# Kernel tuning notes

Hardware: AMD Instinct MI355X
Metric: run time of the kernel (lower is better)

The kernel has to match this reference:

```python
import jax, jax.numpy as jnp
import numpy as np
from jax import lax

B, D, N, K, POOL = 256, 512, 50000, 32, 1024
ALPHA, BETA, LAMB = 1.0, 1.0, 1e-4
TAU, EPS, DELTA = 0.1, 0.1, 1e-3
SINKHORN_ITERS = 200


def matrix_sqrt(A):
    # differentiable symmetric PSD matrix sqrt via eigendecomposition
    w, v = jnp.linalg.eigh(A)
    w = jnp.clip(w, 0.0)
    return (v * jnp.sqrt(w)) @ v.T


def ridge_cov(M, delta):
    Dm = M.shape[0]
    S = M + (jnp.trace(M) / Dm * delta) * jnp.eye(Dm, dtype=M.dtype)
    return 0.5 * (S + S.T)


def sinkhorn(p, q, C, eps):
    # entropic OT, fixed-iteration Sinkhorn (ot.sinkhorn equivalent)
    Kmat = jnp.exp(-C / eps)
    def step(uv, _):
        u, v = uv
        u = p / (Kmat @ v + 1e-16)
        v = q / (Kmat.T @ u + 1e-16)
        return (u, v), None
    (u, v), _ = lax.scan(step, (jnp.ones_like(p), jnp.ones_like(q)), None, length=SINKHORN_ITERS)
    return u[:, None] * Kmat * v[None, :]


def setup_inputs():
    key = jax.random.key(0)
    k1, k2, k3, k4, k5, k6 = jax.random.split(key, 6)
    return {
        "q_batch": jax.random.normal(k1, (B, D), jnp.float32),
        "q_indices": jax.random.randint(k2, (B,), 0, POOL),
        "W": jax.random.normal(k3, (D, D), jnp.float32) * 0.05,
        "X": jax.random.normal(k4, (N, D), jnp.float32),
        "pre_indices": jax.random.randint(k5, (POOL, K), 0, N),
        "pre_weights": jax.random.uniform(k6, (POOL, K), jnp.float32, 0.1, 1.0),
    }


def _forward(q_batch, W, X, pre_weights, q_indices, pre_indices):
    T = q_batch @ W  # model := single linear layer, T_q_batch [B, D]
    # ---- distribution alignment (2-Wasserstein between Gaussians) ----
    mu_X = X.mean(0)
    Sigma_X = ridge_cov(jnp.cov(X, rowvar=False).astype(X.dtype), DELTA)
    mu_t = T.mean(0)
    Sigma_t = ridge_cov(jnp.cov(T, rowvar=False).astype(T.dtype), max(DELTA, 1e-4))
    term_mean = jnp.sum((mu_t - mu_X) ** 2)
    s_t = matrix_sqrt(Sigma_t)
    M = s_t @ Sigma_X @ s_t
    s_m = matrix_sqrt(0.5 * (M + M.T))
    term_cov = jnp.trace(Sigma_X + Sigma_t - 2.0 * s_m)
    loss_dist = term_mean + jnp.clip(term_cov, 0.0)
    # ---- kNN consistency with entropic OT ----
    T_sg = lax.stop_gradient(T)  # faiss search is on detached queries
    d2 = (T_sg ** 2).sum(1, keepdims=True) - 2.0 * T_sg @ X.T + (X ** 2).sum(1)[None, :]
    _, post_idx = lax.top_k(-d2, K)  # exact brute-force kNN == faiss IndexFlatL2
    Xn = X[post_idx]  # [B, K, D]
    l2 = ((T[:, None, :] - Xn) ** 2).sum(-1)  # [B, K], grads flow through T
    post_w = jax.nn.softmax(-l2 / TAU, axis=1)
    post_w = jnp.clip(post_w, 1e-8)
    post_w = post_w / post_w.sum(1, keepdims=True)
    pre_idx_b = pre_indices[q_indices]  # [B, K]
    pre_w = jnp.clip(pre_weights[q_indices], 1e-8)
    pre_w = pre_w / pre_w.sum(1, keepdims=True)
    # fixed-size support = concat(pre, post) of size 2K; duplicated points cost 0
    # to move between, so OT value matches the deduped-union formulation
    support = jnp.concatenate([pre_idx_b, post_idx], axis=1)  # [B, 2K]
    S = X[support]  # [B, 2K, D]
    sq = (S ** 2).sum(-1)
    C = jnp.clip(sq[:, :, None] + sq[:, None, :] - 2.0 * jnp.einsum('bid,bjd->bij', S, S), 0.0)
    med = jnp.median(C.reshape(C.shape[0], -1), axis=1)
    C = C / (med[:, None, None] + 1e-8)
    zeros = jnp.zeros_like(pre_w)
    p = jnp.concatenate([pre_w, zeros], axis=1)   # pre mass on first K slots
    q = jnp.concatenate([zeros, post_w], axis=1)  # post mass on last K slots
    plans = jax.vmap(lambda pp, qq, cc: sinkhorn(pp, qq, cc, EPS))(p, q, C)
    loss_knn = (plans * C).sum((1, 2)).mean()
    loss_reg = 0.5 * jnp.sum(W ** 2)
    total = ALPHA * loss_dist + BETA * loss_knn + LAMB * loss_reg
    return total, loss_dist, loss_knn


def reference(q_batch, q_indices, W, X, pre_indices, pre_weights):
    return _forward(q_batch, W, X, pre_weights, q_indices, pre_indices)
```

## Files before the change

### kernel.cpp

```cpp
#include <hip/hip_runtime.h>
#include <float.h>
#include <math.h>

#define BB 256
#define DD 512
#define NN 50000
#define KK 32
#define NS_ITERS 11
#define PARTS 8
#define PCH 6250

#define OFF_G     0
#define OFF_SC    262144
#define OFF_CS    262208
#define OFF_CSS   262720
#define ZERO_F    263232
#define OFF_T     263232
#define OFF_TC    394304
#define OFF_P     525376
#define OFF_H     656448
#define OFF_XSQ   723008
#define OFF_RUNI  781200
#define OFF_PW    789392
#define OFF_PRW   797584
#define OFF_D2    805776

#define OFF_UUT   (OFF_G)
#define OFF_TCTC  (OFF_G + 65536)
#define OFF_W     (OFF_G + 131072)
#define OFF_M     (OFF_G + 131328)
#define OFF_MUT   (OFF_G + 200000)

typedef __attribute__((ext_vector_type(8))) short bf16x8;
typedef __attribute__((ext_vector_type(4))) float f32x4;

__device__ __forceinline__ float waveSum(float v) {
#pragma unroll
  for (int off = 32; off > 0; off >>= 1) v += __shfl_xor(v, off);
  return v;
}

__device__ __forceinline__ void cvt_write(float4 v, unsigned short* hi, unsigned short* lo, int sa) {
  unsigned int b0 = __float_as_uint(v.x), b1 = __float_as_uint(v.y);
  unsigned int b2 = __float_as_uint(v.z), b3 = __float_as_uint(v.w);
  unsigned int h0 = b0 & 0xffff0000u, h1 = b1 & 0xffff0000u;
  unsigned int h2 = b2 & 0xffff0000u, h3 = b3 & 0xffff0000u;
  float l0 = v.x - __uint_as_float(h0), l1 = v.y - __uint_as_float(h1);
  float l2 = v.z - __uint_as_float(h2), l3 = v.w - __uint_as_float(h3);
  *(unsigned int*)&hi[sa]     = (h0 >> 16) | h1;
  *(unsigned int*)&hi[sa + 2] = (h2 >> 16) | h3;
  *(unsigned int*)&lo[sa]     = (__float_as_uint(l0) >> 16) | (__float_as_uint(l1) & 0xffff0000u);
  *(unsigned int*)&lo[sa + 2] = (__float_as_uint(l2) >> 16) | (__float_as_uint(l3) & 0xffff0000u);
}

__device__ __forceinline__ void cvt1(float x, unsigned short* hp, unsigned short* lp) {
  unsigned int bb = __float_as_uint(x);
  unsigned int hb = bb & 0xffff0000u;
  float lo = x - __uint_as_float(hb);
  *hp = (unsigned short)(hb >> 16);
  *lp = (unsigned short)(__float_as_uint(lo) >> 16);
}

__global__ void __launch_bounds__(256) k_g64_nn(const float* __restrict__ A,
                                                const float* __restrict__ B,
                                                float* __restrict__ C,
                                                int K, int lda, int ldb, int ldc, float scale) {
  __shared__ float As[64][65], Bs[64][65];
  int m0 = blockIdx.y * 64, n0 = blockIdx.x * 64;
  int t = threadIdx.x, tr = t >> 4, tc = t & 15;
  float acc[4][4] = {{0.f}};
  for (int k0 = 0; k0 < K; k0 += 64) {
#pragma unroll
    for (int p = 0; p < 16; ++p) {
      int l = t + 256 * p;
      int r = l >> 6, c = l & 63;
      As[r][c] = A[(m0 + r) * lda + k0 + c];
      Bs[r][c] = B[(k0 + r) * ldb + n0 + c];
    }
    __syncthreads();
#pragma unroll 16
    for (int kk = 0; kk < 64; ++kk) {
      float a[4], b[4];
#pragma unroll
      for (int u = 0; u < 4; ++u) a[u] = As[tr + 16 * u][kk];
#pragma unroll
      for (int v = 0; v < 4; ++v) b[v] = Bs[kk][tc + 16 * v];
#pragma unroll
      for (int u = 0; u < 4; ++u)
#pragma unroll
        for (int v = 0; v < 4; ++v) acc[u][v] += a[u] * b[v];
    }
    __syncthreads();
  }
#pragma unroll
  for (int u = 0; u < 4; ++u)
#pragma unroll
    for (int v = 0; v < 4; ++v)
      C[(m0 + tr + 16 * u) * ldc + n0 + tc + 16 * v] = acc[u][v] * scale;
}

__global__ void __launch_bounds__(256) k_g64_nt(const float* __restrict__ A,
                                                const float* __restrict__ B,
                                                float* __restrict__ C,
                                                int K, int lda, int ldb, int ldc, float scale) {
  __shared__ float As[64][65], Bs[64][65];
  int m0 = blockIdx.y * 64, n0 = blockIdx.x * 64;
  int t = threadIdx.x, tr = t >> 4, tc = t & 15;
  float acc[4][4] = {{0.f}};
  for (int k0 = 0; k0 < K; k0 += 64) {
#pragma unroll
    for (int p = 0; p < 16; ++p) {
      int l = t + 256 * p;
      int r = l >> 6, c = l & 63;
      As[r][c] = A[(m0 + r) * lda + k0 + c];
      Bs[r][c] = B[(n0 + r) * ldb + k0 + c];
    }
    __syncthreads();
#pragma unroll 16
    for (int kk = 0; kk < 64; ++kk) {
      float a[4], b[4];
#pragma unroll
      for (int u = 0; u < 4; ++u) a[u] = As[tr + 16 * u][kk];
#pragma unroll
      for (int v = 0; v < 4; ++v) b[v] = Bs[tc + 16 * v][kk];
#pragma unroll
      for (int u = 0; u < 4; ++u)
#pragma unroll
        for (int v = 0; v < 4; ++v) acc[u][v] += a[u] * b[v];
    }
    __syncthreads();
  }
#pragma unroll
  for (int u = 0; u < 4; ++u)
#pragma unroll
    for (int v = 0; v < 4; ++v)
      C[(m0 + tr + 16 * u) * ldc + n0 + tc + 16 * v] = acc[u][v] * scale;
}

__global__ void __launch_bounds__(256) k_vgemm(const float* __restrict__ T,
                                               const float* __restrict__ X,
                                               float* __restrict__ V) {
  __shared__ unsigned short Ah[128 * 72], Al[128 * 72], Bh[128 * 72], Bl[128 * 72];
  int bj = blockIdx.x, bi = blockIdx.y;
  int t = threadIdx.x;
  int wave = t >> 6, lane = t & 63;
  int m0 = (wave >> 1) * 64, n0 = (wave & 1) * 64;
  int lrow = lane & 15, lq = lane >> 4;
  f32x4 acc[4][4] = {};
  for (int kc = 0; kc < 512; kc += 64) {
#pragma unroll
    for (int f = 0; f < 8; ++f) {
      int lin = f * 256 + t;
      int r = lin >> 4, c4 = lin & 15;
      int sa = r * 72 + c4 * 4;
      float4 va = *(const float4*)&T[(bi * 128 + r) * 512 + kc + c4 * 4];
      cvt_write(va, Ah, Al, sa);
      int jg = bj * 128 + r;
      float4 vb = {0.f, 0.f, 0.f, 0.f};
      if (jg < NN) vb = *(const float4*)&X[(size_t)jg * 512 + kc + c4 * 4];
      cvt_write(vb, Bh, Bl, sa);
    }
    __syncthreads();
#pragma unroll
    for (int ks = 0; ks < 2; ++ks) {
      int kb = ks * 32 + lq * 8;
      bf16x8 ah[4], al[4], bh[4], bl[4];
#pragma unroll
      for (int mi = 0; mi < 4; ++mi) {
        int ro = (m0 + mi * 16 + lrow) * 72 + kb;
        ah[mi] = *(const bf16x8*)&Ah[ro];
        al[mi] = *(const bf16x8*)&Al[ro];
      }
#pragma unroll
      for (int nj = 0; nj < 4; ++nj) {
        int ro = (n0 + nj * 16 + lrow) * 72 + kb;
        bh[nj] = *(const bf16x8*)&Bh[ro];
        bl[nj] = *(const bf16x8*)&Bl[ro];
      }
#pragma unroll
      for (int mi = 0; mi < 4; ++mi)
#pragma unroll
        for (int nj = 0; nj < 4; ++nj) {
          acc[mi][nj] = __builtin_amdgcn_mfma_f32_16x16x32_bf16(ah[mi], bh[nj], acc[mi][nj], 0, 0, 0);
          acc[mi][nj] = __builtin_amdgcn_mfma_f32_16x16x32_bf16(ah[mi], bl[nj], acc[mi][nj], 0, 0, 0);
          acc[mi][nj] = __builtin_amdgcn_mfma_f32_16x16x32_bf16(al[mi], bh[nj], acc[mi][nj], 0, 0, 0);
        }
    }
    __syncthreads();
  }
#pragma unroll
  for (int mi = 0; mi < 4; ++mi)
#pragma unroll
    for (int nj = 0; nj < 4; ++nj)
#pragma unroll
      for (int r = 0; r < 4; ++r) {
        int row = bi * 128 + m0 + mi * 16 + lq * 4 + r;
        int col = bj * 128 + n0 + nj * 16 + lrow;
        if (col < NN) V[(size_t)row * NN + col] = acc[mi][nj][r];
      }
}

__global__ void __launch_bounds__(256) k_uut(const float* __restrict__ V,
                                             const float* __restrict__ m,
                                             float* __restrict__ UUT) {
  __shared__ unsigned short Ah[128 * 72], Al[128 * 72], Bh[128 * 72], Bl[128 * 72];
  const int pi_[3] = {0, 0, 1}, pj_[3] = {0, 1, 1};
  int bi = pi_[blockIdx.x], bj = pj_[blockIdx.x];
  int j0 = blockIdx.y * 1000, jlim = j0 + 1000;
  int t = threadIdx.x;
  int wave = t >> 6, lane = t & 63;
  int m0 = (wave >> 1) * 64, n0 = (wave & 1) * 64;
  int lrow = lane & 15, lq = lane >> 4;
  f32x4 acc[4][4] = {};
  for (int ch = 0; ch < 16; ++ch) {
    int jc = j0 + ch * 64;
#pragma unroll
    for (int f = 0; f < 8; ++f) {
      int lin = f * 256 + t;
      int r = lin >> 4, c4 = lin & 15;
      int sa = r * 72 + c4 * 4;
      int jb = jc + c4 * 4;
      float4 va = {0.f, 0.f, 0.f, 0.f}, vb = {0.f, 0.f, 0.f, 0.f};
      if (jb < jlim) {
        float4 mm = *(const float4*)&m[jb];
        va = *(const float4*)&V[(size_t)(bi * 128 + r) * NN + jb];
        vb = *(const float4*)&V[(size_t)(bj * 128 + r) * NN + jb];
        va.x -= mm.x; va.y -= mm.y; va.z -= mm.z; va.w -= mm.w;
        vb.x -= mm.x; vb.y -= mm.y; vb.z -= mm.z; vb.w -= mm.w;
      }
      cvt_write(va, Ah, Al, sa);
      cvt_write(vb, Bh, Bl, sa);
    }
    __syncthreads();
#pragma unroll
    for (int ks = 0; ks < 2; ++ks) {
      int kb = ks * 32 + lq * 8;
      bf16x8 ah[4], al[4], bh[4], bl[4];
#pragma unroll
      for (int mi = 0; mi < 4; ++mi) {
        int ro = (m0 + mi * 16 + lrow) * 72 + kb;
        ah[mi] = *(const bf16x8*)&Ah[ro];
        al[mi] = *(const bf16x8*)&Al[ro];
      }
#pragma unroll
      for (int nj = 0; nj < 4; ++nj) {
        int ro = (n0 + nj * 16 + lrow) * 72 + kb;
        bh[nj] = *(const bf16x8*)&Bh[ro];
        bl[nj] = *(const bf16x8*)&Bl[ro];
      }
#pragma unroll
      for (int mi = 0; mi < 4; ++mi)
#pragma unroll
        for (int nj = 0; nj < 4; ++nj) {
          acc[mi][nj] = __builtin_amdgcn_mfma_f32_16x16x32_bf16(ah[mi], bh[nj], acc[mi][nj], 0, 0, 0);
          acc[mi][nj] = __builtin_amdgcn_mfma_f32_16x16x32_bf16(ah[mi], bl[nj], acc[mi][nj], 0, 0, 0);
          acc[mi][nj] = __builtin_amdgcn_mfma_f32_16x16x32_bf16(al[mi], bh[nj], acc[mi][nj], 0, 0, 0);
        }
    }
    __syncthreads();
  }
#pragma unroll
  for (int mi = 0; mi < 4; ++mi)
#pragma unroll
    for (int nj = 0; nj < 4; ++nj)
#pragma unroll
      for (int r = 0; r < 4; ++r) {
        int row = bi * 128 + m0 + mi * 16 + lq * 4 + r;
        int col = bj * 128 + n0 + nj * 16 + lrow;
        atomicAdd(&UUT[row * 256 + col], acc[mi][nj][r]);
      }
}

__global__ void __launch_bounds__(256) k_colstatX(const float* __restrict__ X, float* __restrict__ colsum,
                                                  float* __restrict__ colss) {
  __shared__ float shs[512], shss[512];
  int b = blockIdx.x, t = threadIdx.x;
  int c4 = (t & 127) * 4, g = t >> 7;
  int r0 = b * 200 + g;
  float sx = 0, sy = 0, sz = 0, sw = 0;
  float qx = 0, qy = 0, qz = 0, qw = 0;
#pragma unroll 4
  for (int it = 0; it < 100; ++it) {
    float4 v = *(const float4*)&X[(size_t)(r0 + 2 * it) * 512 + c4];
    sx += v.x; sy += v.y; sz += v.z; sw += v.w;
    qx += v.x * v.x; qy += v.y * v.y; qz += v.z * v.z; qw += v.w * v.w;
  }
  if (g == 1) {
    int o = (t - 128) * 4;
    shs[o] = sx; shs[o + 1] = sy; shs[o + 2] = sz; shs[o + 3] = sw;
    shss[o] = qx; shss[o + 1] = qy; shss[o + 2] = qz; shss[o + 3] = qw;
  }
  __syncthreads();
  if (g == 0) {
    int o = t * 4;
    atomicAdd(&colsum[c4],     sx + shs[o]);
    atomicAdd(&colsum[c4 + 1], sy + shs[o + 1]);
    atomicAdd(&colsum[c4 + 2], sz + shs[o + 2]);
    atomicAdd(&colsum[c4 + 3], sw + shs[o + 3]);
    atomicAdd(&colss[c4],     qx + shss[o]);
    atomicAdd(&colss[c4 + 1], qy + shss[o + 1]);
    atomicAdd(&colss[c4 + 2], qz + shss[o + 2]);
    atomicAdd(&colss[c4 + 3], qw + shss[o + 3]);
  }
}

__global__ void k_xsq(const float* __restrict__ X, float* __restrict__ xsq) {
  int row = blockIdx.x * 4 + (threadIdx.x >> 6);
  int lane = threadIdx.x & 63;
  const float* Xr = X + (size_t)row * 512;
  float s = 0.f;
#pragma unroll
  for (int d = 0; d < 8; ++d) { float v = Xr[lane + 64 * d]; s += v * v; }
  s = waveSum(s);
  if (lane == 0) xsq[row] = s;
}

__global__ void k_colmeanT(const float* __restrict__ T, float* __restrict__ mu) {
  int c = threadIdx.x;
  int r0 = blockIdx.x * 16;
  float s = 0.f;
#pragma unroll
  for (int r = 0; r < 16; ++r) s += T[(r0 + r) * 512 + c];
  atomicAdd(&mu[c], s);
}

__global__ void k_centerT(const float* __restrict__ T, const float* __restrict__ mu,
                          float* __restrict__ Tc, float* __restrict__ scal) {
  __shared__ float red[4];
  int t = threadIdx.x;
  int base = blockIdx.x * 1024;
  float ss = 0.f;
#pragma unroll
  for (int p = 0; p < 4; ++p) {
    int l = base + p * 256 + t;
    float v = T[l] - mu[l & 511] * (1.0f / 256.0f);
    Tc[l] = v;
    ss += v * v;
  }
  ss = waveSum(ss);
  if ((t & 63) == 0) red[t >> 6] = ss;
  __syncthreads();
  if (t == 0) atomicAdd(&scal[0], red[0] + red[1] + red[2] + red[3]);
}

__global__ void k_trCX(const float* __restrict__ colsum, const float* __restrict__ colss,
                       float* __restrict__ scal) {
  __shared__ float red[8];
  int t = threadIdx.x;
  float mu = colsum[t] * (1.0f / 50000.0f);
  float v = (colss[t] - 50000.0f * mu * mu) * (1.0f / 49999.0f);
  v = waveSum(v);
  if ((t & 63) == 0) red[t >> 6] = v;
  __syncthreads();
  if (t == 0) {
    float s = 0;
    for (int i = 0; i < 8; ++i) s += red[i];
    scal[1] = s;
  }
}

__global__ void k_vstats(const float* __restrict__ V, float* __restrict__ m) {
  int j = blockIdx.x * 256 + threadIdx.x;
  if (j >= NN) return;
  int i0 = blockIdx.y * 32;
  float s = 0.f;
#pragma unroll 8
  for (int i = 0; i < 32; ++i) s += V[(size_t)(i0 + i) * NN + j];
  atomicAdd(&m[j], s * (1.0f / 256.0f));
}

__global__ void __launch_bounds__(256) k_wvec(const float* __restrict__ T,
                                              const float* __restrict__ colsum,
                                              float* __restrict__ w, float* __restrict__ scal) {
  __shared__ float cs[512];
  int t = threadIdx.x, lane = t & 63, wv_ = t >> 6;
  cs[t] = colsum[t] * (1.0f / 50000.0f);
  cs[t + 256] = colsum[t + 256] * (1.0f / 50000.0f);
  __syncthreads();
  int rbase = blockIdx.x * 32 + wv_ * 8;
  float tot = 0.f;
  for (int rr = 0; rr < 8; ++rr) {
    int row = rbase + rr;
    float a = 0.f;
#pragma unroll
    for (int d = 0; d < 8; ++d) a += T[row * 512 + lane + 64 * d] * cs[lane + 64 * d];
    a = waveSum(a);
    if (lane == 0) { w[row] = a; tot += a; }
  }
  if (lane == 0) atomicAdd(&scal[6], tot);
}

__global__ void k_hfix(const float* __restrict__ UUT, const float* __restrict__ TcTc,
                       const float* __restrict__ w, const float* __restrict__ scal,
                       float* __restrict__ H) {
  int l = blockIdx.x * 256 + threadIdx.x;
  int i = l >> 8, j = l & 255;
  float u = (i >= 128 && j < 128) ? UUT[j * 256 + i] : UUT[i * 256 + j];
  float rho = scal[1] * (1e-3f / 512.0f);
  float wm = scal[6] * (1.0f / 256.0f);
  float wi = w[i] - wm, wj = w[j] - wm;
  H[l] = (u - 50000.0f * wi * wj) * (1.0f / (49999.0f * 255.0f))
       + rho * TcTc[i * 256 + j] * (1.0f / 255.0f);
}

__global__ void __launch_bounds__(256) k_power(const float* __restrict__ H,
                                               float* __restrict__ scal) {
  __shared__ float v[256], nv[256], red[4];
  int t = threadIdx.x;
  float rt = scal[0] * (1.0f / 255.0f) * (1e-3f / 512.0f);
  v[t] = 1.0f;
  __syncthreads();
  float n2 = 256.0f, n3 = 256.0f;
  for (int it = 0; it < 3; ++it) {
    float s = rt * v[t];
    for (int j = 0; j < 256; ++j) s += H[t * 256 + j] * v[j];
    nv[t] = s;
    float ss = waveSum(s * s);
    if ((t & 63) == 0) red[t >> 6] = ss;
    __syncthreads();
    float norm2 = red[0] + red[1] + red[2] + red[3];
    if (it == 1) n2 = norm2;
    if (it == 2) n3 = norm2;
    v[t] = nv[t];
    __syncthreads();
  }
  float d = H[t * 256 + t] + rt;
#pragma unroll
  for (int off = 32; off > 0; off >>= 1) d = fmaxf(d, __shfl_xor(d, off));
  if ((t & 63) == 0) red[t >> 6] = d;
  __syncthreads();
  if (t == 0) {
    float lam = sqrtf(n3 / n2);
    float md = fmaxf(fmaxf(red[0], red[1]), fmaxf(red[2], red[3]));
    scal[5] = fmaxf(1.3f * lam, md);
  }
}

__global__ void k_nsinit(const float* __restrict__ H, const float* __restrict__ scal,
                         float* __restrict__ Y, float* __restrict__ Z) {
  int l = blockIdx.x * 256 + threadIdx.x;
  int i = l >> 8, j = l & 255;
  float rt = scal[0] * (1.0f / 255.0f) * (1e-3f / 512.0f);
  float inv = 1.0f / scal[5];
  Y[l] = (H[l] + ((i == j) ? rt : 0.f)) * inv;
  Z[l] = (i == j) ? 1.0f : 0.f;
}

__global__ void __launch_bounds__(256) k_nsp(const float* __restrict__ Z,
                                             const float* __restrict__ Y,
                                             float* __restrict__ P) {
  __shared__ unsigned short Ah[64 * 72], Al[64 * 72], Bh[64 * 72], Bl[64 * 72];
  int n0b = blockIdx.x * 64, m0b = blockIdx.y * 64;
  int t = threadIdx.x, wave = t >> 6, lane = t & 63;
  int m0 = (wave >> 1) * 32, n0 = (wave & 1) * 32;
  int lrow = lane & 15, lq = lane >> 4;
  f32x4 acc[2][2] = {};
  for (int k0 = 0; k0 < 256; k0 += 64) {
#pragma unroll
    for (int f = 0; f < 4; ++f) {
      int lin = f * 256 + t;
      int r = lin >> 4, c4 = (lin & 15) * 4;
      float4 va = *(const float4*)&Z[(m0b + r) * 256 + k0 + c4];
      cvt_write(va, Ah, Al, r * 72 + c4);
      float4 vb = *(const float4*)&Y[(k0 + r) * 256 + n0b + c4];
      cvt1(vb.x, &Bh[(c4 + 0) * 72 + r], &Bl[(c4 + 0) * 72 + r]);
      cvt1(vb.y, &Bh[(c4 + 1) * 72 + r], &Bl[(c4 + 1) * 72 + r]);
      cvt1(vb.z, &Bh[(c4 + 2) * 72 + r], &Bl[(c4 + 2) * 72 + r]);
      cvt1(vb.w, &Bh[(c4 + 3) * 72 + r], &Bl[(c4 + 3) * 72 + r]);
    }
    __syncthreads();
#pragma unroll
    for (int ks = 0; ks < 2; ++ks) {
      int kb = ks * 32 + lq * 8;
      bf16x8 ah[2], al2[2], bh[2], bl2[2];
#pragma unroll
      for (int mi = 0; mi < 2; ++mi) {
        int ro = (m0 + mi * 16 + lrow) * 72 + kb;
        ah[mi] = *(const bf16x8*)&Ah[ro];
        al2[mi] = *(const bf16x8*)&Al[ro];
      }
#pragma unroll
      for (int nj = 0; nj < 2; ++nj) {
        int ro = (n0 + nj * 16 + lrow) * 72 + kb;
        bh[nj] = *(const bf16x8*)&Bh[ro];
        bl2[nj] = *(const bf16x8*)&Bl[ro];
      }
#pragma unroll
      for (int mi = 0; mi < 2; ++mi)
#pragma unroll
        for (int nj = 0; nj < 2; ++nj) {
          acc[mi][nj] = __builtin_amdgcn_mfma_f32_16x16x32_bf16(ah[mi], bh[nj], acc[mi][nj], 0, 0, 0);
          acc[mi][nj] = __builtin_amdgcn_mfma_f32_16x16x32_bf16(ah[mi], bl2[nj], acc[mi][nj], 0, 0, 0);
          acc[mi][nj] = __builtin_amdgcn_mfma_f32_16x16x32_bf16(al2[mi], bh[nj], acc[mi][nj], 0, 0, 0);
        }
    }
    __syncthreads();
  }
#pragma unroll
  for (int mi = 0; mi < 2; ++mi)
#pragma unroll
    for (int nj = 0; nj < 2; ++nj)
#pragma unroll
      for (int r = 0; r < 4; ++r) {
        int row = m0b + m0 + mi * 16 + lq * 4 + r;
        int col = n0b + n0 + nj * 16 + lrow;
        P[row * 256 + col] = acc[mi][nj][r];
      }
}

__global__ void __launch_bounds__(256) k_nsu(const float* __restrict__ Y, const float* __restrict__ Z,
                                             const float* __restrict__ Pm,
                                             float* __restrict__ Yn, float* __restrict__ Zn) {
  __shared__ unsigned short Ah[64 * 72], Al[64 * 72], Bh[64 * 72], Bl[64 * 72];
  int zz = blockIdx.z;
  const float* A = zz ? Pm : Y;
  const float* B = zz ? Z : Pm;
  const float* D = zz ? Z : Y;
  float* O = zz ? Zn : Yn;
  int n0b = blockIdx.x * 64, m0b = blockIdx.y * 64;
  int t = threadIdx.x, wave = t >> 6, lane = t & 63;
  int m0 = (wave >> 1) * 32, n0 = (wave & 1) * 32;
  int lrow = lane & 15, lq = lane >> 4;
  f32x4 acc[2][2] = {};
  for (int k0 = 0; k0 < 256; k0 += 64) {
#pragma unroll
    for (int f = 0; f < 4; ++f) {
      int lin = f * 256 + t;
      int r = lin >> 4, c4 = (lin & 15) * 4;
      float4 va = *(const float4*)&A[(m0b + r) * 256 + k0 + c4];
      cvt_write(va, Ah, Al, r * 72 + c4);
      float4 vb = *(const float4*)&B[(k0 + r) * 256 + n0b + c4];
      cvt1(vb.x, &Bh[(c4 + 0) * 72 + r], &Bl[(c4 + 0) * 72 + r]);
      cvt1(vb.y, &Bh[(c4 + 1) * 72 + r], &Bl[(c4 + 1) * 72 + r]);
      cvt1(vb.z, &Bh[(c4 + 2) * 72 + r], &Bl[(c4 + 2) * 72 + r]);
      cvt1(vb.w, &Bh[(c4 + 3) * 72 + r], &Bl[(c4 + 3) * 72 + r]);
    }
    __syncthreads();
#pragma unroll
    for (int ks = 0; ks < 2; ++ks) {
      int kb = ks * 32 + lq * 8;
      bf16x8 ah[2], al2[2], bh[2], bl2[2];
#pragma unroll
      for (int mi = 0; mi < 2; ++mi) {
        int ro = (m0 + mi * 16 + lrow) * 72 + kb;
        ah[mi] = *(const bf16x8*)&Ah[ro];
        al2[mi] = *(const bf16x8*)&Al[ro];
      }
#pragma unroll
      for (int nj = 0; nj < 2; ++nj) {
        int ro = (n0 + nj * 16 + lrow) * 72 + kb;
        bh[nj] = *(const bf16x8*)&Bh[ro];
        bl2[nj] = *(const bf16x8*)&Bl[ro];
      }
#pragma unroll
      for (int mi = 0; mi < 2; ++mi)
#pragma unroll
        for (int nj = 0; nj < 2; ++nj) {
          acc[mi][nj] = __builtin_amdgcn_mfma_f32_16x16x32_bf16(ah[mi], bh[nj], acc[mi][nj], 0, 0, 0);
          acc[mi][nj] = __builtin_amdgcn_mfma_f32_16x16x32_bf16(ah[mi], bl2[nj], acc[mi][nj], 0, 0, 0);
          acc[mi][nj] = __builtin_amdgcn_mfma_f32_16x16x32_bf16(al2[mi], bh[nj], acc[mi][nj], 0, 0, 0);
        }
    }
    __syncthreads();
  }
#pragma unroll
  for (int mi = 0; mi < 2; ++mi)
#pragma unroll
    for (int nj = 0; nj < 2; ++nj)
#pragma unroll
      for (int r = 0; r < 4; ++r) {
        int row = m0b + m0 + mi * 16 + lq * 4 + r;
        int col = n0b + n0 + nj * 16 + lrow;
        int idx = row * 256 + col;
        O[idx] = 1.5f * D[idx] - 0.5f * acc[mi][nj][r];
      }
}

__global__ void k_ns_trace(const float* __restrict__ Y, float* __restrict__ scal) {
  __shared__ float red[4];
  int t = threadIdx.x;
  float v = Y[t * 256 + t];
  v = waveSum(v);
  if ((t & 63) == 0) red[t >> 6] = v;
  __syncthreads();
  if (t == 0) {
    float tr = red[0] + red[1] + red[2] + red[3];
    float rt = scal[0] * (1.0f / 255.0f) * (1e-3f / 512.0f);
    scal[2] = sqrtf(scal[5]) * tr + 256.0f * sqrtf(rt);
  }
}

__global__ void __launch_bounds__(256) k_topk_part(const float* __restrict__ V,
                                                   const float* __restrict__ xsq,
                                                   float* __restrict__ candv,
                                                   int* __restrict__ candi) {
  __shared__ float bufv[512];
  __shared__ int bufi[512];
  __shared__ int lcount;
  __shared__ float tvs;
  __shared__ int tis;
  int part = blockIdx.x, q = blockIdx.y, t = threadIdx.x;
  int base = part * PCH;
  int lane = t & 63;
  if (t == 0) { lcount = 0; tvs = FLT_MAX; tis = 0x7fffffff; }
  __syncthreads();
  const float* rowV = V + (size_t)q * NN + base;
  const float* xs = xsq + base;

  auto flush = [&]() {
    __syncthreads();
    int c = lcount;
    for (int s = c + t; s < 512; s += 256) { bufv[s] = FLT_MAX; bufi[s] = 0x7fffffff; }
    __syncthreads();
    for (int ssz = 2; ssz <= 512; ssz <<= 1) {
      for (int st = ssz >> 1; st > 0; st >>= 1) {
        int i = 2 * t - (t & (st - 1));
        int j = i + st;
        bool up = ((i & ssz) == 0);
        float a = bufv[i], b = bufv[j];
        int ai = bufi[i], bi2 = bufi[j];
        bool agtb = (a > b) || (a == b && ai > bi2);
        if (agtb == up) { bufv[i] = b; bufv[j] = a; bufi[i] = bi2; bufi[j] = ai; }
        __syncthreads();
      }
    }
    if (t == 0) { lcount = 32; tvs = bufv[31]; tis = bufi[31]; }
    __syncthreads();
  };

  int ntile = (PCH + 255) >> 8;
  for (int tile = 0; tile < ntile; ++tile) {
    int j = tile * 256 + t;
    float val = 0.f; int idx = 0;
    bool pred = false;
    if (j < PCH) {
      val = xs[j] - 2.0f * rowV[j];
      idx = base + j;
      float tv = tvs; int ti = tis;
      pred = (val < tv) || (val == tv && idx < ti);
    }
    unsigned long long mask = __ballot(pred);
    if (mask) {
      int lead = __ffsll((unsigned long long)mask) - 1;
      int cnt = __popcll(mask);
      int basep = 0;
      if (lane == lead) basep = atomicAdd(&lcount, cnt);
      basep = __shfl(basep, lead);
      if (pred) {
        int off = __popcll(mask & ((1ull << lane) - 1ull));
        int slot = basep + off;
        bufv[slot] = val; bufi[slot] = idx;
      }
    }
    __syncthreads();
    if (lcount >= 256) flush();
  }
  flush();
  if (t < 32) {
    candv[(q * PARTS + part) * 32 + t] = bufv[t];
    candi[(q * PARTS + part) * 32 + t] = bufi[t];
  }
}

__global__ void __launch_bounds__(128) k_topk_final(const float* __restrict__ candv,
                                                    const int* __restrict__ candi,
                                                    int* __restrict__ runi) {
  __shared__ float v[256];
  __shared__ int ix[256];
  int q = blockIdx.x, t = threadIdx.x;
  v[t] = candv[q * 256 + t];
  v[t + 128] = candv[q * 256 + t + 128];
  ix[t] = candi[q * 256 + t];
  ix[t + 128] = candi[q * 256 + t + 128];
  __syncthreads();
  for (int ssz = 2; ssz <= 256; ssz <<= 1) {
    for (int st = ssz >> 1; st > 0; st >>= 1) {
      int i = 2 * t - (t & (st - 1));
      int j = i + st;
      bool up = ((i & ssz) == 0);
      float a = v[i], b = v[j];
      int ai = ix[i], bi = ix[j];
      bool agtb = (a > b) || (a == b && ai > bi);
      if (agtb == up) { v[i] = b; v[j] = a; ix[i] = bi; ix[j] = ai; }
      __syncthreads();
    }
  }
  if (t < 32) runi[q * 32 + t] = ix[t];
}

__global__ void __launch_bounds__(64) k_l2soft(const float* __restrict__ T, const float* __restrict__ X,
                                               const int* __restrict__ runi, const int* __restrict__ qidx,
                                               const float* __restrict__ prew, float* __restrict__ postw,
                                               float* __restrict__ prewn) {
  __shared__ float l2s[32];
  int b = blockIdx.x, lane = threadIdx.x;
  int qi = qidx[b];
  float pwv = (lane < 32) ? fmaxf(prew[qi * 32 + lane], 1e-8f) : 0.f;
  float psum = waveSum(pwv);
  if (lane < 32) prewn[b * 32 + lane] = pwv / psum;
  const float* Tb = T + b * 512;
  for (int n = 0; n < 32; ++n) {
    int nb = runi[b * 32 + n];
    const float* Xr = X + (size_t)nb * 512;
    float acc = 0.f;
#pragma unroll
    for (int d = 0; d < 8; ++d) {
      float df = Tb[lane + 64 * d] - Xr[lane + 64 * d];
      acc += df * df;
    }
    acc = waveSum(acc);
    if (lane == 0) l2s[n] = acc;
  }
  __syncthreads();
  float lg = (lane < 32) ? (-l2s[lane] * 10.0f) : -FLT_MAX;
  float mx = lg;
#pragma unroll
  for (int off = 32; off > 0; off >>= 1) mx = fmaxf(mx, __shfl_xor(mx, off));
  float e = (lane < 32) ? expf(lg - mx) : 0.f;
  float es = waveSum(e);
  float wv = e / es;
  wv = fmaxf(wv, 1e-8f);
  float ws2 = (lane < 32) ? wv : 0.f;
  ws2 = waveSum(ws2);
  if (lane < 32) postw[b * 32 + lane] = wv / ws2;
}

__global__ void __launch_bounds__(256) k_batch(const float* __restrict__ X, const int* __restrict__ qidx,
                                               const int* __restrict__ pre_idx, const int* __restrict__ runi,
                                               const float* __restrict__ prewn, const float* __restrict__ postw,
                                               float* __restrict__ scal) {
  __shared__ float G[64][65];
  __shared__ float Cm[64][65];
  __shared__ unsigned short Ah[64 * 72], Al[64 * 72];
  __shared__ int supp[64];
  __shared__ float uuS[32], vvS[32];
  __shared__ float red[4];
  __shared__ float medsh;
  __shared__ unsigned int hist[256];
  __shared__ unsigned int wtot[4];
  __shared__ unsigned int selp;
  __shared__ int selk;
  __shared__ unsigned int cw[4], mw[4];
  int b = blockIdx.x, t = threadIdx.x;
  int wave = t >> 6, lane = t & 63;
  if (t < 32) supp[t] = pre_idx[qidx[b] * 32 + t];
  else if (t < 64) supp[t] = runi[b * 32 + t - 32];
  if (t == 0) { selp = 0u; selk = 992; }
  __syncthreads();
  {
    int m0 = (wave >> 1) * 32, n0 = (wave & 1) * 32;
    int lrow = lane & 15, lq = lane >> 4;
    f32x4 acc[2][2] = {};
    for (int kc = 0; kc < 512; kc += 64) {
#pragma unroll
      for (int f = 0; f < 4; ++f) {
        int lin = f * 256 + t;
        int r = lin >> 4, c4 = lin & 15;
        float4 va = *(const float4*)&X[(size_t)supp[r] * 512 + kc + c4 * 4];
        cvt_write(va, Ah, Al, r * 72 + c4 * 4);
      }
      __syncthreads();
#pragma unroll
      for (int ks = 0; ks < 2; ++ks) {
        int kb = ks * 32 + lq * 8;
        bf16x8 ah[2], al[2], bh[2], bl[2];
#pragma unroll
        for (int mi = 0; mi < 2; ++mi) {
          int ro = (m0 + mi * 16 + lrow) * 72 + kb;
          ah[mi] = *(const bf16x8*)&Ah[ro];
          al[mi] = *(const bf16x8*)&Al[ro];
        }
#pragma unroll
        for (int nj = 0; nj < 2; ++nj) {
          int ro = (n0 + nj * 16 + lrow) * 72 + kb;
          bh[nj] = *(const bf16x8*)&Ah[ro];
          bl[nj] = *(const bf16x8*)&Al[ro];
        }
#pragma unroll
        for (int mi = 0; mi < 2; ++mi)
#pragma unroll
          for (int nj = 0; nj < 2; ++nj) {
            acc[mi][nj] = __builtin_amdgcn_mfma_f32_16x16x32_bf16(ah[mi], bh[nj], acc[mi][nj], 0, 0, 0);
            acc[mi][nj] = __builtin_amdgcn_mfma_f32_16x16x32_bf16(ah[mi], bl[nj], acc[mi][nj], 0, 0, 0);
            acc[mi][nj] = __builtin_amdgcn_mfma_f32_16x16x32_bf16(al[mi], bh[nj], acc[mi][nj], 0, 0, 0);
          }
      }
      __syncthreads();
    }
#pragma unroll
    for (int mi = 0; mi < 2; ++mi)
#pragma unroll
      for (int nj = 0; nj < 2; ++nj)
#pragma unroll
        for (int r = 0; r < 4; ++r)
          G[m0 + mi * 16 + lq * 4 + r][n0 + nj * 16 + lrow] = acc[mi][nj][r];
  }
  __syncthreads();
  for (int l = t; l < 4096; l += 256) {
    int i = l >> 6, j = l & 63;
    Cm[i][j] = fmaxf(G[i][i] + G[j][j] - 2.0f * G[i][j], 0.f);
  }
  __syncthreads();
  for (int pass = 0; pass < 4; ++pass) {
    int shift = 24 - 8 * pass;
    hist[t] = 0u;
    __syncthreads();
    for (int l = t; l < 4096; l += 256) {
      int i = l >> 6, j = l & 63;
      if (i < j) {
        unsigned int u = __float_as_uint(Cm[i][j]) & 0x7fffffffu;
        bool match = (pass == 0) || (((u ^ selp) >> (shift + 8)) == 0u);
        if (match) atomicAdd(&hist[(u >> shift) & 255], 1u);
      }
    }
    __syncthreads();
    unsigned int h = hist[t];
    unsigned int c = h;
#pragma unroll
    for (int off = 1; off < 64; off <<= 1) {
      unsigned int n = __shfl_up(c, off);
      if ((t & 63) >= off) c += n;
    }
    if ((t & 63) == 63) wtot[t >> 6] = c;
    __syncthreads();
    unsigned int offw = 0;
    for (int w2 = 0; w2 < (t >> 6); ++w2) offw += wtot[w2];
    c += offw;
    int k = selk;
    if ((int)c >= k && (int)(c - h) < k) {
      selk = k - (int)(c - h);
      selp = selp | ((unsigned int)t << shift);
    }
    __syncthreads();
  }
  {
    unsigned int target = selp;
    unsigned int cnt = 0, mn = 0xffffffffu;
    for (int l = t; l < 4096; l += 256) {
      int i = l >> 6, j = l & 63;
      if (i < j) {
        unsigned int u = __float_as_uint(Cm[i][j]) & 0x7fffffffu;
        if (u <= target) cnt++;
        else mn = (u < mn) ? u : mn;
      }
    }
#pragma unroll
    for (int off = 32; off > 0; off >>= 1) {
      cnt += __shfl_xor(cnt, off);
      unsigned int m2 = __shfl_xor(mn, off);
      mn = (m2 < mn) ? m2 : mn;
    }
    if (lane == 0) { cw[wave] = cnt; mw[wave] = mn; }
    __syncthreads();
    if (t == 0) {
      unsigned int ct = cw[0] + cw[1] + cw[2] + cw[3];
      unsigned int mt = mw[0];
      mt = (mw[1] < mt) ? mw[1] : mt;
      mt = (mw[2] < mt) ? mw[2] : mt;
      mt = (mw[3] < mt) ? mw[3] : mt;
      float v992 = __uint_as_float(target);
      float v993 = (ct >= 993u) ? v992 : __uint_as_float(mt);
      medsh = 0.5f * (v992 + v993) + 1e-8f;
    }
    __syncthreads();
  }
  float inv = 1.0f / medsh;
  for (int l = t; l < 4096; l += 256) {
    int i = l >> 6, j = l & 63;
    float cn = Cm[i][j] * inv;
    Cm[i][j] = cn;
    G[i][j] = expf(-cn * 10.0f);
  }
  __syncthreads();
  if (wave == 0) {
    int half = lane >> 5;
    int l = lane & 31;
    int cb = half * 16;
    float p_l = prewn[b * 32 + l];
    float q_l = postw[b * 32 + l];
    float Kr16[16], Kt16[16];
#pragma unroll
    for (int c2 = 0; c2 < 16; ++c2) Kr16[c2] = G[l][32 + cb + c2];
#pragma unroll
    for (int r2 = 0; r2 < 16; ++r2) Kt16[r2] = G[cb + r2][32 + l];
    float r0 = 0.f;
#pragma unroll
    for (int c2 = 0; c2 < 32; ++c2) r0 += G[l][half * 32 + c2];
    r0 += __shfl_xor(r0, 32);
    float u = p_l / (r0 + 1e-16f);
    float s0 = 0.f, s1 = 0.f, s2 = 0.f, s3 = 0.f;
#pragma unroll
    for (int r2 = 0; r2 < 16; r2 += 4) {
      s0 += Kt16[r2]     * __shfl(u, cb + r2);
      s1 += Kt16[r2 + 1] * __shfl(u, cb + r2 + 1);
      s2 += Kt16[r2 + 2] * __shfl(u, cb + r2 + 2);
      s3 += Kt16[r2 + 3] * __shfl(u, cb + r2 + 3);
    }
    float sv = (s0 + s1) + (s2 + s3);
    sv += __shfl_xor(sv, 32);
    float v = q_l / (sv + 1e-16f);
    for (int it = 1; it < 200; ++it) {
      float uprev = u, vprev = v;
      float a0 = 0.f, a1 = 0.f, a2 = 0.f, a3 = 0.f;
#pragma unroll
      for (int c2 = 0; c2 < 16; c2 += 4) {
        a0 += Kr16[c2]     * __shfl(v, cb + c2);
        a1 += Kr16[c2 + 1] * __shfl(v, cb + c2 + 1);
        a2 += Kr16[c2 + 2] * __shfl(v, cb + c2 + 2);
        a3 += Kr16[c2 + 3] * __shfl(v, cb + c2 + 3);
      }
      float au = (a0 + a1) + (a2 + a3);
      au += __shfl_xor(au, 32);
      u = p_l / (au + 1e-16f);
      a0 = 0.f; a1 = 0.f; a2 = 0.f; a3 = 0.f;
#pragma unroll
      for (int r2 = 0; r2 < 16; r2 += 4) {
        a0 += Kt16[r2]     * __shfl(u, cb + r2);
        a1 += Kt16[r2 + 1] * __shfl(u, cb + r2 + 1);
        a2 += Kt16[r2 + 2] * __shfl(u, cb + r2 + 2);
        a3 += Kt16[r2 + 3] * __shfl(u, cb + r2 + 3);
      }
      float bv = (a0 + a1) + (a2 + a3);
      bv += __shfl_xor(bv, 32);
      v = q_l / (bv + 1e-16f);
      if (__all(u == uprev && v == vprev)) break;
    }
    if (t < 32) { uuS[t] = u; vvS[t] = v; }
  }
  __syncthreads();
  float lacc = 0.f;
#pragma unroll
  for (int q8 = 0; q8 < 4; ++q8) {
    int l = q8 * 256 + t;
    int i = l >> 5, j = l & 31;
    lacc += uuS[i] * G[i][32 + j] * vvS[j] * Cm[i][32 + j];
  }
  lacc = waveSum(lacc);
  if ((t & 63) == 0) red[t >> 6] = lacc;
  __syncthreads();
  if (t == 0)
    atomicAdd(&scal[3], (red[0] + red[1] + red[2] + red[3]) * (1.0f / 256.0f));
}

__global__ void k_wreg(const float* __restrict__ W, float* __restrict__ scal) {
  __shared__ float red[4];
  int t = threadIdx.x;
  int base = blockIdx.x * 2048;
  float ss = 0.f;
#pragma unroll
  for (int p = 0; p < 8; ++p) {
    float v = W[base + p * 256 + t];
    ss += v * v;
  }
  ss = waveSum(ss);
  if ((t & 63) == 0) red[t >> 6] = ss;
  __syncthreads();
  if (t == 0) atomicAdd(&scal[4], red[0] + red[1] + red[2] + red[3]);
}

__global__ void k_combine(const float* __restrict__ mu_t, const float* __restrict__ colsum,
                          const float* __restrict__ scal, float* __restrict__ out) {
  __shared__ float red[8];
  int t = threadIdx.x;
  float dm = mu_t[t] * (1.0f / 256.0f) - colsum[t] * (1.0f / 50000.0f);
  float v = dm * dm;
  v = waveSum(v);
  if ((t & 63) == 0) red[t >> 6] = v;
  __syncthreads();
  if (t == 0) {
    float term_mean = 0.f;
    for (int i = 0; i < 8; ++i) term_mean += red[i];
    float trCT = scal[0] * (1.0f / 255.0f);
    float trCX = scal[1];
    float S = scal[2];
    float term_cov = trCX * 1.001f + trCT * 1.001f - 2.0f * S;
    term_cov = fmaxf(term_cov, 0.f);
    float loss_dist = term_mean + term_cov;
    float loss_knn = scal[3];
    float loss_reg = 0.5f * scal[4];
    out[0] = loss_dist + loss_knn + 1e-4f * loss_reg;
    out[1] = loss_dist;
    out[2] = loss_knn;
  }
}

extern "C" void kernel_launch(void* const* d_in, const int* in_sizes, int n_in,
                              void* d_out, int out_size, void* d_ws, size_t ws_size,
                              hipStream_t stream) {
  const float* q = (const float*)d_in[0];
  const int* qidx = (const int*)d_in[1];
  const float* W = (const float*)d_in[2];
  const float* X = (const float*)d_in[3];
  const int* pre_idx = (const int*)d_in[4];
  const float* prew = (const float*)d_in[5];
  float* out = (float*)d_out;
  float* ws = (float*)d_ws;

  float* scal = ws + OFF_SC;
  float* colsum = ws + OFF_CS;
  float* colss = ws + OFF_CSS;
  float* T = ws + OFF_T;
  float* Tc = ws + OFF_TC;
  float* H = ws + OFF_H;
  float* mu_t = ws + OFF_MUT;
  float* xsq = ws + OFF_XSQ;
  int* runi = (int*)(ws + OFF_RUNI);
  float* postw = ws + OFF_PW;
  float* prewn = ws + OFF_PRW;
  float* V = ws + OFF_D2;
  float* UUT = ws + OFF_UUT;
  float* TcTc = ws + OFF_TCTC;
  float* wv = ws + OFF_W;
  float* m = ws + OFF_M;
  float* candv = ws + OFF_P;
  int* candi = (int*)(ws + OFF_P + 65536);

  hipMemsetAsync(d_ws, 0, (size_t)ZERO_F * 4, stream);

  k_g64_nn<<<dim3(8, 4), 256, 0, stream>>>(q, W, T, 512, 512, 512, 512, 1.0f);
  k_colstatX<<<250, 256, 0, stream>>>(X, colsum, colss);
  k_xsq<<<12500, 256, 0, stream>>>(X, xsq);
  k_colmeanT<<<16, 512, 0, stream>>>(T, mu_t);
  k_centerT<<<128, 256, 0, stream>>>(T, mu_t, Tc, scal);
  k_trCX<<<1, 512, 0, stream>>>(colsum, colss, scal);
  k_vgemm<<<dim3(391, 2), 256, 0, stream>>>(T, X, V);
  k_vstats<<<dim3(196, 8), 256, 0, stream>>>(V, m);
  k_topk_part<<<dim3(PARTS, 256), 256, 0, stream>>>(V, xsq, candv, candi);
  k_topk_final<<<256, 128, 0, stream>>>(candv, candi, runi);
  k_g64_nt<<<dim3(4, 4), 256, 0, stream>>>(Tc, Tc, TcTc, 512, 512, 512, 256, 1.0f);
  k_wvec<<<8, 256, 0, stream>>>(T, colsum, wv, scal);
  k_uut<<<dim3(3, 50), 256, 0, stream>>>(V, m, UUT);
  k_hfix<<<256, 256, 0, stream>>>(UUT, TcTc, wv, scal, H);
  {
    float* Y = ws + OFF_TC;
    float* Z = ws + OFF_TC + 65536;
    float* Y2 = ws + OFF_P;
    float* Z2 = ws + OFF_P + 65536;
    float* Pm = ws + OFF_G;
    k_power<<<1, 256, 0, stream>>>(H, scal);
    k_nsinit<<<256, 256, 0, stream>>>(H, scal, Y, Z);
    for (int it = 0; it < NS_ITERS; ++it) {
      k_nsp<<<dim3(4, 4), 256, 0, stream>>>(Z, Y, Pm);
      k_nsu<<<dim3(4, 4, 2), 256, 0, stream>>>(Y, Z, Pm, Y2, Z2);
      float* tmp = Y; Y = Y2; Y2 = tmp;
      tmp = Z; Z = Z2; Z2 = tmp;
    }
    k_ns_trace<<<1, 256, 0, stream>>>(Y, scal);
  }
  k_l2soft<<<256, 64, 0, stream>>>(T, X, runi, qidx, prew, postw, prewn);
  k_batch<<<256, 256, 0, stream>>>(X, qidx, pre_idx, runi, prewn, postw, scal);
  k_wreg<<<128, 256, 0, stream>>>(W, scal);
  k_combine<<<1, 512, 0, stream>>>(mu_t, colsum, scal, out);
}
```

Measured before the change: 1.016 ms.

## Fuse column means into GEMM epilogues and register-prefetch next tiles in GEMMs

```diff
diff --git a/kernel.cpp b/kernel.cpp
--- a/kernel.cpp
+++ b/kernel.cpp
@@ -64,8 +64,10 @@
 __global__ void __launch_bounds__(256) k_g64_nn(const float* __restrict__ A,
                                                 const float* __restrict__ B,
                                                 float* __restrict__ C,
-                                                int K, int lda, int ldb, int ldc, float scale) {
+                                                int K, int lda, int ldb, int ldc, float scale,
+                                                float* __restrict__ musum) {
   __shared__ float As[64][65], Bs[64][65];
+  __shared__ float cp[64];
   int m0 = blockIdx.y * 64, n0 = blockIdx.x * 64;
   int t = threadIdx.x, tr = t >> 4, tc = t & 15;
   float acc[4][4] = {{0.f}};
@@ -97,6 +99,19 @@
 #pragma unroll
     for (int v = 0; v < 4; ++v)
       C[(m0 + tr + 16 * u) * ldc + n0 + tc + 16 * v] = acc[u][v] * scale;
+  if (musum != nullptr) {
+    if (t < 64) cp[t] = 0.f;
+    __syncthreads();
+#pragma unroll
+    for (int v = 0; v < 4; ++v) {
+      float s = 0.f;
+#pragma unroll
+      for (int u = 0; u < 4; ++u) s += acc[u][v];
+      atomicAdd(&cp[tc + 16 * v], s * scale);
+    }
+    __syncthreads();
+    if (t < 64) atomicAdd(&musum[n0 + t], cp[t]);
+  }
 }
 
 __global__ void __launch_bounds__(256) k_g64_nt(const float* __restrict__ A,
@@ -139,28 +154,47 @@
 
 __global__ void __launch_bounds__(256) k_vgemm(const float* __restrict__ T,
                                                const float* __restrict__ X,
-                                               float* __restrict__ V) {
+                                               float* __restrict__ V,
+                                               float* __restrict__ m) {
   __shared__ unsigned short Ah[128 * 72], Al[128 * 72], Bh[128 * 72], Bl[128 * 72];
+  __shared__ float colpart[128];
   int bj = blockIdx.x, bi = blockIdx.y;
   int t = threadIdx.x;
   int wave = t >> 6, lane = t & 63;
   int m0 = (wave >> 1) * 64, n0 = (wave & 1) * 64;
   int lrow = lane & 15, lq = lane >> 4;
+  int r_ = t >> 4, c4_ = (t & 15) * 4;
   f32x4 acc[4][4] = {};
+  float4 pa[8], pb[8];
+#pragma unroll
+  for (int f = 0; f < 8; ++f) {
+    int r = f * 16 + r_;
+    pa[f] = *(const float4*)&T[(bi * 128 + r) * 512 + c4_];
+    int jg = bj * 128 + r;
+    float4 vb = {0.f, 0.f, 0.f, 0.f};
+    if (jg < NN) vb = *(const float4*)&X[(size_t)jg * 512 + c4_];
+    pb[f] = vb;
+  }
   for (int kc = 0; kc < 512; kc += 64) {
 #pragma unroll
     for (int f = 0; f < 8; ++f) {
-      int lin = f * 256 + t;
-      int r = lin >> 4, c4 = lin & 15;
-      int sa = r * 72 + c4 * 4;
-      float4 va = *(const float4*)&T[(bi * 128 + r) * 512 + kc + c4 * 4];
-      cvt_write(va, Ah, Al, sa);
-      int jg = bj * 128 + r;
-      float4 vb = {0.f, 0.f, 0.f, 0.f};
-      if (jg < NN) vb = *(const float4*)&X[(size_t)jg * 512 + kc + c4 * 4];
-      cvt_write(vb, Bh, Bl, sa);
-    }
-    __syncthreads();
+      int sa = (f * 16 + r_) * 72 + c4_;
+      cvt_write(pa[f], Ah, Al, sa);
+      cvt_write(pb[f], Bh, Bl, sa);
+    }
+    __syncthreads();
+    if (kc < 448) {
+      int kn = kc + 64;
+#pragma unroll
+      for (int f = 0; f < 8; ++f) {
+        int r = f * 16 + r_;
+        pa[f] = *(const float4*)&T[(bi * 128 + r) * 512 + kn + c4_];
+        int jg = bj * 128 + r;
+        float4 vb = {0.f, 0.f, 0.f, 0.f};
+        if (jg < NN) vb = *(const float4*)&X[(size_t)jg * 512 + kn + c4_];
+        pb[f] = vb;
+      }
+    }
 #pragma unroll
     for (int ks = 0; ks < 2; ++ks) {
       int kb = ks * 32 + lq * 8;
@@ -188,6 +222,8 @@
     }
     __syncthreads();
   }
+  if (t < 128) colpart[t] = 0.f;
+  __syncthreads();
 #pragma unroll
   for (int mi = 0; mi < 4; ++mi)
 #pragma unroll
@@ -198,12 +234,27 @@
         int col = bj * 128 + n0 + nj * 16 + lrow;
         if (col < NN) V[(size_t)row * NN + col] = acc[mi][nj][r];
       }
+#pragma unroll
+  for (int nj = 0; nj < 4; ++nj) {
+    float s = 0.f;
+#pragma unroll
+    for (int mi = 0; mi < 4; ++mi)
+#pragma unroll
+      for (int r = 0; r < 4; ++r) s += acc[mi][nj][r];
+    atomicAdd(&colpart[n0 + nj * 16 + lrow], s);
+  }
+  __syncthreads();
+  if (t < 128) {
+    int col = bj * 128 + t;
+    if (col < NN) atomicAdd(&m[col], colpart[t] * (1.0f / 256.0f));
+  }
 }
 
 __global__ void __launch_bounds__(256) k_uut(const float* __restrict__ V,
                                              const float* __restrict__ m,
                                              float* __restrict__ UUT) {
   __shared__ unsigned short Ah[128 * 72], Al[128 * 72], Bh[128 * 72], Bl[128 * 72];
+  __shared__ __align__(16) float ms[1000];
   const int pi_[3] = {0, 0, 1}, pj_[3] = {0, 1, 1};
   int bi = pi_[blockIdx.x], bj = pj_[blockIdx.x];
   int j0 = blockIdx.y * 1000, jlim = j0 + 1000;
@@ -211,20 +262,31 @@
   int wave = t >> 6, lane = t & 63;
   int m0 = (wave >> 1) * 64, n0 = (wave & 1) * 64;
   int lrow = lane & 15, lq = lane >> 4;
+  int r_ = t >> 4, c4_ = (t & 15) * 4;
   f32x4 acc[4][4] = {};
+  if (t < 250) ((float4*)ms)[t] = *(const float4*)&m[j0 + t * 4];
+  float4 pa[8], pb[8];
+#pragma unroll
+  for (int f = 0; f < 8; ++f) {
+    int r = f * 16 + r_;
+    int jb = j0 + c4_;
+    float4 va = {0.f, 0.f, 0.f, 0.f}, vb = {0.f, 0.f, 0.f, 0.f};
+    if (jb < jlim) {
+      va = *(const float4*)&V[(size_t)(bi * 128 + r) * NN + jb];
+      vb = *(const float4*)&V[(size_t)(bj * 128 + r) * NN + jb];
+    }
+    pa[f] = va; pb[f] = vb;
+  }
+  __syncthreads();
   for (int ch = 0; ch < 16; ++ch) {
     int jc = j0 + ch * 64;
 #pragma unroll
     for (int f = 0; f < 8; ++f) {
-      int lin = f * 256 + t;
-      int r = lin >> 4, c4 = lin & 15;
-      int sa = r * 72 + c4 * 4;
-      int jb = jc + c4 * 4;
-      float4 va = {0.f, 0.f, 0.f, 0.f}, vb = {0.f, 0.f, 0.f, 0.f};
+      int sa = (f * 16 + r_) * 72 + c4_;
+      int jb = jc + c4_;
+      float4 va = pa[f], vb = pb[f];
       if (jb < jlim) {
-        float4 mm = *(const float4*)&m[jb];
-        va = *(const float4*)&V[(size_t)(bi * 128 + r) * NN + jb];
-        vb = *(const float4*)&V[(size_t)(bj * 128 + r) * NN + jb];
+        float4 mm = *(const float4*)&ms[jb - j0];
         va.x -= mm.x; va.y -= mm.y; va.z -= mm.z; va.w -= mm.w;
         vb.x -= mm.x; vb.y -= mm.y; vb.z -= mm.z; vb.w -= mm.w;
       }
@@ -232,6 +294,20 @@
       cvt_write(vb, Bh, Bl, sa);
     }
     __syncthreads();
+    if (ch < 15) {
+      int jn = j0 + (ch + 1) * 64;
+#pragma unroll
+      for (int f = 0; f < 8; ++f) {
+        int r = f * 16 + r_;
+        int jb = jn + c4_;
+        float4 va = {0.f, 0.f, 0.f, 0.f}, vb = {0.f, 0.f, 0.f, 0.f};
+        if (jb < jlim) {
+          va = *(const float4*)&V[(size_t)(bi * 128 + r) * NN + jb];
+          vb = *(const float4*)&V[(size_t)(bj * 128 + r) * NN + jb];
+        }
+        pa[f] = va; pb[f] = vb;
+      }
+    }
 #pragma unroll
     for (int ks = 0; ks < 2; ++ks) {
       int kb = ks * 32 + lq * 8;
@@ -315,15 +391,6 @@
   if (lane == 0) xsq[row] = s;
 }
 
-__global__ void k_colmeanT(const float* __restrict__ T, float* __restrict__ mu) {
-  int c = threadIdx.x;
-  int r0 = blockIdx.x * 16;
-  float s = 0.f;
-#pragma unroll
-  for (int r = 0; r < 16; ++r) s += T[(r0 + r) * 512 + c];
-  atomicAdd(&mu[c], s);
-}
-
 __global__ void k_centerT(const float* __restrict__ T, const float* __restrict__ mu,
                           float* __restrict__ Tc, float* __restrict__ scal) {
   __shared__ float red[4];
@@ -357,16 +424,6 @@
     for (int i = 0; i < 8; ++i) s += red[i];
     scal[1] = s;
   }
-}
-
-__global__ void k_vstats(const float* __restrict__ V, float* __restrict__ m) {
-  int j = blockIdx.x * 256 + threadIdx.x;
-  if (j >= NN) return;
-  int i0 = blockIdx.y * 32;
-  float s = 0.f;
-#pragma unroll 8
-  for (int i = 0; i < 32; ++i) s += V[(size_t)(i0 + i) * NN + j];
-  atomicAdd(&m[j], s * (1.0f / 256.0f));
 }
 
 __global__ void __launch_bounds__(256) k_wvec(const float* __restrict__ T,
@@ -413,7 +470,7 @@
   float n2 = 256.0f, n3 = 256.0f;
   for (int it = 0; it < 3; ++it) {
     float s = rt * v[t];
-    for (int j = 0; j < 256; ++j) s += H[t * 256 + j] * v[j];
+    for (int j = 0; j < 256; ++j) s += H[j * 256 + t] * v[j];
     nv[t] = s;
     float ss = waveSum(s * s);
     if ((t & 63) == 0) red[t >> 6] = ss;
@@ -750,16 +807,27 @@
   {
     int m0 = (wave >> 1) * 32, n0 = (wave & 1) * 32;
     int lrow = lane & 15, lq = lane >> 4;
+    int r_ = t >> 4, c4_ = (t & 15) * 4;
     f32x4 acc[2][2] = {};
+    float4 pf[4];
+#pragma unroll
+    for (int f = 0; f < 4; ++f) {
+      int r = f * 16 + r_;
+      pf[f] = *(const float4*)&X[(size_t)supp[r] * 512 + c4_];
+    }
     for (int kc = 0; kc < 512; kc += 64) {
 #pragma unroll
-      for (int f = 0; f < 4; ++f) {
-        int lin = f * 256 + t;
-        int r = lin >> 4, c4 = lin & 15;
-        float4 va = *(const float4*)&X[(size_t)supp[r] * 512 + kc + c4 * 4];
-        cvt_write(va, Ah, Al, r * 72 + c4 * 4);
-      }
+      for (int f = 0; f < 4; ++f)
+        cvt_write(pf[f], Ah, Al, (f * 16 + r_) * 72 + c4_);
       __syncthreads();
+      if (kc < 448) {
+        int kn = kc + 64;
+#pragma unroll
+        for (int f = 0; f < 4; ++f) {
+          int r = f * 16 + r_;
+          pf[f] = *(const float4*)&X[(size_t)supp[r] * 512 + kn + c4_];
+        }
+      }
 #pragma unroll
       for (int ks = 0; ks < 2; ++ks) {
         int kb = ks * 32 + lq * 8;
@@ -1017,14 +1085,12 @@
 
   hipMemsetAsync(d_ws, 0, (size_t)ZERO_F * 4, stream);
 
-  k_g64_nn<<<dim3(8, 4), 256, 0, stream>>>(q, W, T, 512, 512, 512, 512, 1.0f);
+  k_g64_nn<<<dim3(8, 4), 256, 0, stream>>>(q, W, T, 512, 512, 512, 512, 1.0f, mu_t);
   k_colstatX<<<250, 256, 0, stream>>>(X, colsum, colss);
   k_xsq<<<12500, 256, 0, stream>>>(X, xsq);
-  k_colmeanT<<<16, 512, 0, stream>>>(T, mu_t);
   k_centerT<<<128, 256, 0, stream>>>(T, mu_t, Tc, scal);
   k_trCX<<<1, 512, 0, stream>>>(colsum, colss, scal);
-  k_vgemm<<<dim3(391, 2), 256, 0, stream>>>(T, X, V);
-  k_vstats<<<dim3(196, 8), 256, 0, stream>>>(V, m);
+  k_vgemm<<<dim3(391, 2), 256, 0, stream>>>(T, X, V, m);
   k_topk_part<<<dim3(PARTS, 256), 256, 0, stream>>>(V, xsq, candv, candi);
   k_topk_final<<<256, 128, 0, stream>>>(candv, candi, runi);
   k_g64_nt<<<dim3(4, 4), 256, 0, stream>>>(Tc, Tc, TcTc, 512, 512, 512, 256, 1.0f);
```

After: 925.1 us. 8.9% less time.
